# Kernel tuning notes

Measured on AMD Instinct MI355X. Metric: run time of the kernel, lower is better.

## Reference

```python
import jax, jax.numpy as jnp
import numpy as np
from jax import lax


def _dtw_normalized(x, y):
    """DTW with symmetric2 step pattern and cityblock (L1) local cost on scalars.

    D[0,0] = d[0,0]; D[i,0] = D[i-1,0] + d[i,0]; D[0,j] = D[0,j-1] + d[0,j]
    D[i,j] = min(D[i-1,j-1] + 2*d, D[i-1,j] + d, D[i,j-1] + d)
    normalizedDistance = D[n-1,m-1] / (n + m)
    """
    n = x.shape[0]

    def row_update(d_prev, xi):
        d = jnp.abs(xi - y)              # local cost row, [m]
        first = d_prev[0] + d[0]         # D[i,0]

        def step(left, inp):
            dj, up, diag = inp
            val = jnp.minimum(jnp.minimum(diag + 2.0 * dj, up + dj), left + dj)
            return val, val

        _, rest = lax.scan(step, first, (d[1:], d_prev[1:], d_prev[:-1]))
        new_row = jnp.concatenate([first[None], rest])
        return new_row, None

    d0 = jnp.cumsum(jnp.abs(x[0] - y))   # D[0, :]
    d_last, _ = lax.scan(row_update, d0, x[1:])
    return d_last[-1] / (2.0 * n)        # n + m with n == m


def setup_inputs() -> dict:
    key = jax.random.key(0)
    k1, k2 = jax.random.split(key)
    x = jax.random.normal(k1, (64, 1024), dtype=jnp.float32)
    x_target = jax.random.normal(k2, (64, 1024), dtype=jnp.float32)
    return {"x": x, "x_target": x_target}


def reference(x, x_target):
    dists = jax.vmap(_dtw_normalized)(x, x_target)  # [bs]
    return jnp.mean(dists)
```

## Files before the change

kernel.cpp:

```cpp
#include <hip/hip_runtime.h>

#define SEQ_N 1024
#define BATCH 64
#define NW    4
#define RPL   4
#define KSL   16
#define DELTA (64 + KSL)
#define RINGN 80
#define PAD_F 304
#define PAD_B 352

__device__ __forceinline__ float wave_shr1(float v, float fill) {
    return __int_as_float(__builtin_amdgcn_update_dpp(
        __float_as_int(fill), __float_as_int(v), 0x138, 0xF, 0xF, false));
}

__global__ __launch_bounds__(256, 1) void dtw_kernel(const float* __restrict__ x,
                                                     const float* __restrict__ y,
                                                     float* __restrict__ dists) {
    __shared__ float sy_raw[PAD_F + SEQ_N + PAD_B];
    __shared__ float ring[NW - 1][RINGN];

    const int b   = blockIdx.x;
    const int tid = threadIdx.x;
    const int w   = tid >> 6;
    const int l   = tid & 63;
    const float INF = 3.0e37f;
    const int  off = w * DELTA + l;
    const bool is_ring_l0 = (l == 0) && (w > 0);
    const bool is_tid0 = (tid == 0);

    for (int i = tid; i < PAD_F; i += 256) sy_raw[i] = 0.0f;
    for (int i = tid; i < PAD_B; i += 256) sy_raw[PAD_F + SEQ_N + i] = 0.0f;
    ((float4*)(sy_raw + PAD_F))[tid] = ((const float4*)(y + b * SEQ_N))[tid];
    const float4 xv = *((const float4*)(x + b * SEQ_N + w * 256 + l * RPL));
    const float xr0 = xv.x, xr1 = xv.y, xr2 = xv.z, xr3 = xv.w;
    __syncthreads();

    const float* const yp = sy_raw + PAD_F - off;

    float c0 = INF, c1 = INF, c2 = INF, c3 = INF;
    float diag_top = INF, bottom = INF;
    float yA[KSL], yB[KSL], rb[KSL], bt[KSL];

    #pragma unroll
    for (int k = 0; k < KSL; ++k) yA[k] = yp[k];

#define EPOCH(MASKED, FIRST, S0, YU, YF)                                     \
  {                                                                          \
    __syncthreads();                                                         \
    if (w > 0) {                                                             \
      int rbase = ((S0) & 63) + 47; if (rbase >= 64) rbase -= 64;            \
      const float* rp = ring[w - 1] + rbase;                                 \
      _Pragma("unroll")                                                      \
      for (int k2 = 0; k2 < KSL; ++k2) rb[k2] = rp[k2];                      \
    } else {                                                                 \
      _Pragma("unroll")                                                      \
      for (int k2 = 0; k2 < KSL; ++k2) rb[k2] = INF;                         \
    }                                                                        \
    _Pragma("unroll")                                                        \
    for (int k2 = 0; k2 < KSL; ++k2) YF[k2] = yp[(S0) + KSL + k2];           \
    _Pragma("unroll")                                                        \
    for (int k2 = 0; k2 < KSL; ++k2) {                                       \
      const float up_dpp = wave_shr1(bottom, INF);                           \
      float upv = is_ring_l0 ? rb[k2] : up_dpp;                              \
      if ((FIRST) && k2 == 0 && is_tid0) upv = 0.0f;      \
      const float yj = YU[k2];                                               \
      bool act = true;                                                       \
      if (MASKED) act = ((unsigned)((S0) + k2 - off) < (unsigned)SEQ_N);     \
      if (act) {                                                             \
        const float d0 = xr0 - yj, d1 = xr1 - yj,                            \
                    d2 = xr2 - yj, d3 = xr3 - yj;                            \
        const float t0 = diag_top + fabsf(d0);                               \
        const float t1 = c0 + fabsf(d1);                                     \
        const float t2 = c1 + fabsf(d2);                                     \
        const float t3 = c2 + fabsf(d3);                                     \
        float v = upv;                                                       \
        v = fminf(fminf(t0, c0), v) + fabsf(d0); c0 = v;                     \
        v = fminf(fminf(t1, c1), v) + fabsf(d1); c1 = v;                     \
        v = fminf(fminf(t2, c2), v) + fabsf(d2); c2 = v;                     \
        v = fminf(fminf(t3, c3), v) + fabsf(d3); c3 = v;                     \
        diag_top = upv; bottom = v;                                          \
      }                                                                      \
      if ((FIRST) && k2 == 0 && is_tid0) diag_top = INF; \
      bt[k2] = bottom;                                                       \
    }                                                                        \
    if (w < NW - 1 && l == 63) {                                             \
      const int mm = (S0) & 63;                                              \
      float* wp = ring[w] + mm;                                              \
      _Pragma("unroll")                                                      \
      for (int k2 = 0; k2 < KSL; ++k2) wp[k2] = bt[k2];                      \
      if (mm == 0) {                                                         \
        _Pragma("unroll")                                                    \
        for (int k2 = 0; k2 < KSL; ++k2) ring[w][64 + k2] = bt[k2];          \
      }                                                                      \
    }                                                                        \
  }

    EPOCH(true, true, 0, yA, yB);
    EPOCH(true, false, 16, yB, yA);
    int s0 = 32;
    for (int it = 1; it < 10; ++it) {
        EPOCH(true, false, s0, yA, yB);
        EPOCH(true, false, s0 + 16, yB, yA);
        s0 += 32;
    }
    for (int it = 0; it < 22; ++it) {
        EPOCH(false, false, s0, yA, yB);
        EPOCH(false, false, s0 + 16, yB, yA);
        s0 += 32;
    }
    for (int it = 0; it < 10; ++it) {
        EPOCH(true, false, s0, yA, yB);
        EPOCH(true, false, s0 + 16, yB, yA);
        s0 += 32;
    }
#undef EPOCH

    if (tid == 255) dists[b] = c3 * (1.0f / (2.0f * (float)SEQ_N));
}

__global__ void dtw_reduce_kernel(const float* __restrict__ dists,
                                  float* __restrict__ out) {
    float v = dists[threadIdx.x] * (1.0f / (float)BATCH);
    #pragma unroll
    for (int o = 32; o > 0; o >>= 1) v += __shfl_down(v, o);
    if (threadIdx.x == 0) out[0] = v;
}

extern "C" void kernel_launch(void* const* d_in, const int* in_sizes, int n_in,
                              void* d_out, int out_size, void* d_ws, size_t ws_size,
                              hipStream_t stream) {
    const float* x = (const float*)d_in[0];
    const float* y = (const float*)d_in[1];
    float* out = (float*)d_out;
    float* dists = (float*)d_ws;

    dtw_kernel<<<BATCH, 256, 0, stream>>>(x, y, dists);
    dtw_reduce_kernel<<<1, BATCH, 0, stream>>>(dists, out);
}
```

Baseline: 88.70 us.

## Double epoch length and stream ring exchange per step instead of batched

Raises the per-epoch step count from 16 to 32, halving the number of block-wide barriers, and widens the wavefront lag between waves to match. The batched ring reads and writes and the register prefetch of y are replaced by per-step LDS reads and writes into a 128-entry ring, with lane 63 writing each bottom value immediately. This trims register pressure and barrier count, at the cost of extra LDS accesses inside the serial dependency chain and a longer pipeline fill/drain.

```diff
diff --git a/kernel.cpp b/kernel.cpp
--- a/kernel.cpp
+++ b/kernel.cpp
@@ -4,10 +4,11 @@
 #define BATCH 64
 #define NW    4
 #define RPL   4
-#define KSL   16
-#define DELTA (64 + KSL)
-#define RINGN 80
-#define PAD_F 304
+#define KSL   32
+#define DELTA 96
+#define LAG   33
+#define RINGM 128
+#define PAD_F 352
 #define PAD_B 352
 
 __device__ __forceinline__ float wave_shr1(float v, float fill) {
@@ -19,7 +20,7 @@
                                                      const float* __restrict__ y,
                                                      float* __restrict__ dists) {
     __shared__ float sy_raw[PAD_F + SEQ_N + PAD_B];
-    __shared__ float ring[NW - 1][RINGN];
+    __shared__ float ring[NW - 1][RINGM];
 
     const int b   = blockIdx.x;
     const int tid = threadIdx.x;
@@ -27,7 +28,6 @@
     const int l   = tid & 63;
     const float INF = 3.0e37f;
     const int  off = w * DELTA + l;
-    const bool is_ring_l0 = (l == 0) && (w > 0);
     const bool is_tid0 = (tid == 0);
 
     for (int i = tid; i < PAD_F; i += 256) sy_raw[i] = 0.0f;
@@ -41,31 +41,22 @@
 
     float c0 = INF, c1 = INF, c2 = INF, c3 = INF;
     float diag_top = INF, bottom = INF;
-    float yA[KSL], yB[KSL], rb[KSL], bt[KSL];
 
-    #pragma unroll
-    for (int k = 0; k < KSL; ++k) yA[k] = yp[k];
-
-#define EPOCH(MASKED, FIRST, S0, YU, YF)                                     \
+#define EPOCH(MASKED, FIRST, S0)                                             \
   {                                                                          \
     __syncthreads();                                                         \
-    if (w > 0) {                                                             \
-      int rbase = ((S0) & 63) + 47; if (rbase >= 64) rbase -= 64;            \
-      const float* rp = ring[w - 1] + rbase;                                 \
-      _Pragma("unroll")                                                      \
-      for (int k2 = 0; k2 < KSL; ++k2) rb[k2] = rp[k2];                      \
-    } else {                                                                 \
-      _Pragma("unroll")                                                      \
-      for (int k2 = 0; k2 < KSL; ++k2) rb[k2] = INF;                         \
-    }                                                                        \
-    _Pragma("unroll")                                                        \
-    for (int k2 = 0; k2 < KSL; ++k2) YF[k2] = yp[(S0) + KSL + k2];           \
     _Pragma("unroll")                                                        \
     for (int k2 = 0; k2 < KSL; ++k2) {                                       \
       const float up_dpp = wave_shr1(bottom, INF);                           \
-      float upv = is_ring_l0 ? rb[k2] : up_dpp;                              \
+      float upv;                                                             \
+      if (w > 0) {                                                           \
+        const float rv = ring[w - 1][((S0) + k2 - LAG) & (RINGM - 1)];       \
+        upv = (l == 0) ? rv : up_dpp;                                        \
+      } else {                                                               \
+        upv = up_dpp;                                                        \
+      }                                                                      \
       if ((FIRST) && k2 == 0 && is_tid0) upv = 0.0f;      \
-      const float yj = YU[k2];                                               \
+      const float yj = yp[(S0) + k2];                                        \
       bool act = true;                                                       \
       if (MASKED) act = ((unsigned)((S0) + k2 - off) < (unsigned)SEQ_N);     \
       if (act) {                                                             \
@@ -83,38 +74,16 @@
         diag_top = upv; bottom = v;                                          \
       }                                                                      \
       if ((FIRST) && k2 == 0 && is_tid0) diag_top = INF; \
-      bt[k2] = bottom;                                                       \
-    }                                                                        \
-    if (w < NW - 1 && l == 63) {                                             \
-      const int mm = (S0) & 63;                                              \
-      float* wp = ring[w] + mm;                                              \
-      _Pragma("unroll")                                                      \
-      for (int k2 = 0; k2 < KSL; ++k2) wp[k2] = bt[k2];                      \
-      if (mm == 0) {                                                         \
-        _Pragma("unroll")                                                    \
-        for (int k2 = 0; k2 < KSL; ++k2) ring[w][64 + k2] = bt[k2];          \
-      }                                                                      \
+      if (w < NW - 1 && l == 63)                                             \
+        ring[w][((S0) + k2) & (RINGM - 1)] = bottom;                         \
     }                                                                        \
   }
 
-    EPOCH(true, true, 0, yA, yB);
-    EPOCH(true, false, 16, yB, yA);
-    int s0 = 32;
-    for (int it = 1; it < 10; ++it) {
-        EPOCH(true, false, s0, yA, yB);
-        EPOCH(true, false, s0 + 16, yB, yA);
-        s0 += 32;
-    }
-    for (int it = 0; it < 22; ++it) {
-        EPOCH(false, false, s0, yA, yB);
-        EPOCH(false, false, s0 + 16, yB, yA);
-        s0 += 32;
-    }
-    for (int it = 0; it < 10; ++it) {
-        EPOCH(true, false, s0, yA, yB);
-        EPOCH(true, false, s0 + 16, yB, yA);
-        s0 += 32;
-    }
+    int s0 = 0;
+    EPOCH(true, true, 0); s0 = 32;
+    for (int e = 1; e <= 10; ++e) { EPOCH(true, false, s0); s0 += 32; }
+    for (int e = 11; e <= 31; ++e) { EPOCH(false, false, s0); s0 += 32; }
+    for (int e = 32; e <= 42; ++e) { EPOCH(true, false, s0); s0 += 32; }
 #undef EPOCH
 
     if (tid == 255) dists[b] = c3 * (1.0f / (2.0f * (float)SEQ_N));
```

After: 195.7 us. +120.6%, slower.

## Process two DP columns per wavefront step to halve the anti-diagonal steps

Applied to the files above, without the earlier changes.

Each lane now computes two adjacent y-columns (a float2 pair) per step instead of one, so the wavefront sweeps 512 column pairs rather than 1024 columns. Shared y storage and the inter-wave ring buffer become float2, the epoch count drops by about half, and the masking uses the pair index. This cuts the number of DPP shifts, barriers and serial steps. The cost is a longer dependency chain inside each step (eight chained min-adds instead of four) and more registers.

```diff
diff --git a/kernel.cpp b/kernel.cpp
--- a/kernel.cpp
+++ b/kernel.cpp
@@ -3,12 +3,12 @@
 #define SEQ_N 1024
 #define BATCH 64
 #define NW    4
-#define RPL   4
 #define KSL   16
-#define DELTA (64 + KSL)
+#define DELTA 80
 #define RINGN 80
-#define PAD_F 304
-#define PAD_B 352
+#define PAD_F2 304
+#define PAD_B2 320
+#define NPAIR 512
 
 __device__ __forceinline__ float wave_shr1(float v, float fill) {
     return __int_as_float(__builtin_amdgcn_update_dpp(
@@ -18,8 +18,8 @@
 __global__ __launch_bounds__(256, 1) void dtw_kernel(const float* __restrict__ x,
                                                      const float* __restrict__ y,
                                                      float* __restrict__ dists) {
-    __shared__ float sy_raw[PAD_F + SEQ_N + PAD_B];
-    __shared__ float ring[NW - 1][RINGN];
+    __shared__ float2 sy2[PAD_F2 + NPAIR + PAD_B2];
+    __shared__ float2 ring[NW - 1][RINGN];
 
     const int b   = blockIdx.x;
     const int tid = threadIdx.x;
@@ -28,66 +28,77 @@
     const float INF = 3.0e37f;
     const int  off = w * DELTA + l;
     const bool is_ring_l0 = (l == 0) && (w > 0);
-    const bool is_tid0 = (tid == 0);
+    const bool is_seed = (tid == 0);
 
-    for (int i = tid; i < PAD_F; i += 256) sy_raw[i] = 0.0f;
-    for (int i = tid; i < PAD_B; i += 256) sy_raw[PAD_F + SEQ_N + i] = 0.0f;
-    ((float4*)(sy_raw + PAD_F))[tid] = ((const float4*)(y + b * SEQ_N))[tid];
-    const float4 xv = *((const float4*)(x + b * SEQ_N + w * 256 + l * RPL));
+    for (int i = tid; i < PAD_F2; i += 256) sy2[i] = make_float2(0.f, 0.f);
+    for (int i = tid; i < PAD_B2; i += 256) sy2[PAD_F2 + NPAIR + i] = make_float2(0.f, 0.f);
+    ((float4*)(sy2 + PAD_F2))[tid] = ((const float4*)(y + b * SEQ_N))[tid];
+    const float4 xv = *((const float4*)(x + b * SEQ_N + w * 256 + l * 4));
     const float xr0 = xv.x, xr1 = xv.y, xr2 = xv.z, xr3 = xv.w;
     __syncthreads();
 
-    const float* const yp = sy_raw + PAD_F - off;
+    const float2* const yp2 = sy2 + PAD_F2 - off;
 
     float c0 = INF, c1 = INF, c2 = INF, c3 = INF;
-    float diag_top = INF, bottom = INF;
-    float yA[KSL], yB[KSL], rb[KSL], bt[KSL];
+    float diag_top = INF;
+    float botA = INF, botB = INF;
+    float2 yA[KSL], yB[KSL], rb[KSL], bt[KSL];
 
     #pragma unroll
-    for (int k = 0; k < KSL; ++k) yA[k] = yp[k];
+    for (int k = 0; k < KSL; ++k) yA[k] = yp2[k];
+    #pragma unroll
+    for (int k = 0; k < KSL; ++k) rb[k] = make_float2(INF, INF);
 
 #define EPOCH(MASKED, FIRST, S0, YU, YF)                                     \
   {                                                                          \
     __syncthreads();                                                         \
     if (w > 0) {                                                             \
       int rbase = ((S0) & 63) + 47; if (rbase >= 64) rbase -= 64;            \
-      const float* rp = ring[w - 1] + rbase;                                 \
+      const float2* rp = ring[w - 1] + rbase;                                \
       _Pragma("unroll")                                                      \
       for (int k2 = 0; k2 < KSL; ++k2) rb[k2] = rp[k2];                      \
-    } else {                                                                 \
-      _Pragma("unroll")                                                      \
-      for (int k2 = 0; k2 < KSL; ++k2) rb[k2] = INF;                         \
     }                                                                        \
     _Pragma("unroll")                                                        \
-    for (int k2 = 0; k2 < KSL; ++k2) YF[k2] = yp[(S0) + KSL + k2];           \
+    for (int k2 = 0; k2 < KSL; ++k2) YF[k2] = yp2[(S0) + KSL + k2];          \
     _Pragma("unroll")                                                        \
     for (int k2 = 0; k2 < KSL; ++k2) {                                       \
-      const float up_dpp = wave_shr1(bottom, INF);                           \
-      float upv = is_ring_l0 ? rb[k2] : up_dpp;                              \
-      if ((FIRST) && k2 == 0 && is_tid0) upv = 0.0f;      \
-      const float yj = YU[k2];                                               \
+      float upA = wave_shr1(botA, INF);                                      \
+      float upB = wave_shr1(botB, INF);                                      \
+      if (is_ring_l0) { upA = rb[k2].x; upB = rb[k2].y; }                    \
+      const float dgB0 = upA;             \
+      if ((FIRST) && k2 == 0 && is_seed) upA = 0.0f;         \
+      const float2 yv = YU[k2];                                              \
       bool act = true;                                                       \
-      if (MASKED) act = ((unsigned)((S0) + k2 - off) < (unsigned)SEQ_N);     \
+      if (MASKED) act = ((unsigned)((S0) + k2 - off) < (unsigned)NPAIR);     \
       if (act) {                                                             \
-        const float d0 = xr0 - yj, d1 = xr1 - yj,                            \
-                    d2 = xr2 - yj, d3 = xr3 - yj;                            \
-        const float t0 = diag_top + fabsf(d0);                               \
-        const float t1 = c0 + fabsf(d1);                                     \
-        const float t2 = c1 + fabsf(d2);                                     \
-        const float t3 = c2 + fabsf(d3);                                     \
-        float v = upv;                                                       \
-        v = fminf(fminf(t0, c0), v) + fabsf(d0); c0 = v;                     \
-        v = fminf(fminf(t1, c1), v) + fabsf(d1); c1 = v;                     \
-        v = fminf(fminf(t2, c2), v) + fabsf(d2); c2 = v;                     \
-        v = fminf(fminf(t3, c3), v) + fabsf(d3); c3 = v;                     \
-        diag_top = upv; bottom = v;                                          \
+        const float dA0 = xr0 - yv.x, dA1 = xr1 - yv.x,                      \
+                    dA2 = xr2 - yv.x, dA3 = xr3 - yv.x;                      \
+        const float dB0 = xr0 - yv.y, dB1 = xr1 - yv.y,                      \
+                    dB2 = xr2 - yv.y, dB3 = xr3 - yv.y;                      \
+        const float tA0 = diag_top + fabsf(dA0);                             \
+        const float tA1 = c0 + fabsf(dA1);                                   \
+        const float tA2 = c1 + fabsf(dA2);                                   \
+        const float tA3 = c2 + fabsf(dA3);                                   \
+        const float a0 = fminf(fminf(tA0, c0), upA) + fabsf(dA0);            \
+        const float a1 = fminf(fminf(tA1, c1), a0) + fabsf(dA1);             \
+        const float a2 = fminf(fminf(tA2, c2), a1) + fabsf(dA2);             \
+        const float a3 = fminf(fminf(tA3, c3), a2) + fabsf(dA3);             \
+        const float tB0 = dgB0 + fabsf(dB0);                                 \
+        const float tB1 = a0 + fabsf(dB1);                                   \
+        const float tB2 = a1 + fabsf(dB2);                                   \
+        const float tB3 = a2 + fabsf(dB3);                                   \
+        const float b0 = fminf(fminf(tB0, a0), upB) + fabsf(dB0);            \
+        const float b1 = fminf(fminf(tB1, a1), b0) + fabsf(dB1);             \
+        const float b2 = fminf(fminf(tB2, a2), b1) + fabsf(dB2);             \
+        const float b3 = fminf(fminf(tB3, a3), b2) + fabsf(dB3);             \
+        c0 = b0; c1 = b1; c2 = b2; c3 = b3;                                  \
+        diag_top = upB; botA = a3; botB = b3;                                \
       }                                                                      \
-      if ((FIRST) && k2 == 0 && is_tid0) diag_top = INF; \
-      bt[k2] = bottom;                                                       \
+      bt[k2].x = botA; bt[k2].y = botB;                                      \
     }                                                                        \
     if (w < NW - 1 && l == 63) {                                             \
       const int mm = (S0) & 63;                                              \
-      float* wp = ring[w] + mm;                                              \
+      float2* wp = ring[w] + mm;                                             \
       _Pragma("unroll")                                                      \
       for (int k2 = 0; k2 < KSL; ++k2) wp[k2] = bt[k2];                      \
       if (mm == 0) {                                                         \
@@ -98,23 +109,24 @@
   }
 
     EPOCH(true, true, 0, yA, yB);
-    EPOCH(true, false, 16, yB, yA);
-    int s0 = 32;
-    for (int it = 1; it < 10; ++it) {
+    int s0 = 16;
+    for (int it = 0; it < 9; ++it) {
+        EPOCH(true, false, s0, yB, yA);
+        EPOCH(true, false, s0 + 16, yA, yB);
+        s0 += 32;
+    }
+    for (int it = 0; it < 6; ++it) {
+        EPOCH(false, false, s0, yB, yA);
+        EPOCH(false, false, s0 + 16, yA, yB);
+        s0 += 32;
+    }
+    EPOCH(false, false, s0, yB, yA); s0 += 16;
+    for (int it = 0; it < 9; ++it) {
         EPOCH(true, false, s0, yA, yB);
         EPOCH(true, false, s0 + 16, yB, yA);
         s0 += 32;
     }
-    for (int it = 0; it < 22; ++it) {
-        EPOCH(false, false, s0, yA, yB);
-        EPOCH(false, false, s0 + 16, yB, yA);
-        s0 += 32;
-    }
-    for (int it = 0; it < 10; ++it) {
-        EPOCH(true, false, s0, yA, yB);
-        EPOCH(true, false, s0 + 16, yB, yA);
-        s0 += 32;
-    }
+    EPOCH(true, false, s0, yA, yB);
 #undef EPOCH
 
     if (tid == 255) dists[b] = c3 * (1.0f / (2.0f * (float)SEQ_N));
```

Measured after the change: 93.58 us. +5.5%, slower.

## Split DTW into forward and backward half-sweeps meeting at middle column

Applied to the files above, without the earlier changes.

Each block now runs two DTW recurrences at once. One is a forward sweep over the first 512 columns, the other a backward sweep over the reversed sequences for the remaining columns. A new stitch kernel then combines the two boundary columns with a min over rows to recover the full-path cost. This halves the length of the serial anti-diagonal wavefront, which is the critical-path latency, but doubles the ALU work per epoch and adds an extra kernel launch plus workspace traffic. The backward recurrence carries extra local-cost state through the ring buffers, which adds register and LDS pressure.

```diff
diff --git a/kernel.cpp b/kernel.cpp
--- a/kernel.cpp
+++ b/kernel.cpp
@@ -3,23 +3,27 @@
 #define SEQ_N 1024
 #define BATCH 64
 #define NW    4
-#define RPL   4
 #define KSL   16
-#define DELTA (64 + KSL)
+#define DELTA 80
 #define RINGN 80
 #define PAD_F 304
-#define PAD_B 352
+#define PAD_B 320
+#define NPAIR 512
+#define SYN   (PAD_F + NPAIR + PAD_B)
 
 __device__ __forceinline__ float wave_shr1(float v, float fill) {
     return __int_as_float(__builtin_amdgcn_update_dpp(
         __float_as_int(fill), __float_as_int(v), 0x138, 0xF, 0xF, false));
 }
 
-__global__ __launch_bounds__(256, 1) void dtw_kernel(const float* __restrict__ x,
-                                                     const float* __restrict__ y,
-                                                     float* __restrict__ dists) {
-    __shared__ float sy_raw[PAD_F + SEQ_N + PAD_B];
-    __shared__ float ring[NW - 1][RINGN];
+__global__ __launch_bounds__(256, 1) void dtw_fused_kernel(const float* __restrict__ x,
+                                                           const float* __restrict__ y,
+                                                           float* __restrict__ wsF,
+                                                           float* __restrict__ wsP) {
+    __shared__ float  syF[SYN];
+    __shared__ float  syB[SYN];
+    __shared__ float  ringF[NW - 1][RINGN];
+    __shared__ float2 ringB[NW - 1][RINGN];
 
     const int b   = blockIdx.x;
     const int tid = threadIdx.x;
@@ -28,96 +32,174 @@
     const float INF = 3.0e37f;
     const int  off = w * DELTA + l;
     const bool is_ring_l0 = (l == 0) && (w > 0);
-    const bool is_tid0 = (tid == 0);
-
-    for (int i = tid; i < PAD_F; i += 256) sy_raw[i] = 0.0f;
-    for (int i = tid; i < PAD_B; i += 256) sy_raw[PAD_F + SEQ_N + i] = 0.0f;
-    ((float4*)(sy_raw + PAD_F))[tid] = ((const float4*)(y + b * SEQ_N))[tid];
-    const float4 xv = *((const float4*)(x + b * SEQ_N + w * 256 + l * RPL));
-    const float xr0 = xv.x, xr1 = xv.y, xr2 = xv.z, xr3 = xv.w;
+    const bool is_seed = (tid == 0);
+    const int  r0 = w * 256 + l * 4;
+
+    for (int i = tid; i < PAD_F; i += 256) { syF[i] = 0.0f; syB[i] = 0.0f; }
+    for (int i = tid; i < PAD_B; i += 256) {
+        syF[PAD_F + NPAIR + i] = 0.0f; syB[PAD_F + NPAIR + i] = 0.0f;
+    }
+    if (tid < NPAIR / 4) {
+        ((float4*)(syF + PAD_F))[tid] = ((const float4*)(y + b * SEQ_N))[tid];
+        const float4 v = *((const float4*)(y + b * SEQ_N + 1020 - 4 * tid));
+        ((float4*)(syB + PAD_F))[tid] = make_float4(v.w, v.z, v.y, v.x);
+    }
+    const float4 xf = *((const float4*)(x + b * SEQ_N + r0));
+    const float xF0 = xf.x, xF1 = xf.y, xF2 = xf.z, xF3 = xf.w;
+    const float4 xb = *((const float4*)(x + b * SEQ_N + 1020 - r0));
+    const float xB0 = xb.w, xB1 = xb.z, xB2 = xb.y, xB3 = xb.x;
     __syncthreads();
 
-    const float* const yp = sy_raw + PAD_F - off;
+    const float* const ypF = syF + PAD_F - off;
+    const float* const ypB = syB + PAD_F - off;
 
     float c0 = INF, c1 = INF, c2 = INF, c3 = INF;
-    float diag_top = INF, bottom = INF;
-    float yA[KSL], yB[KSL], rb[KSL], bt[KSL];
-
-    #pragma unroll
-    for (int k = 0; k < KSL; ++k) yA[k] = yp[k];
-
-#define EPOCH(MASKED, FIRST, S0, YU, YF)                                     \
+    float diag_top = INF, botF = INF;
+    float cP0 = INF, cP1 = INF, cP2 = INF, cP3 = INF;
+    float cD0 = 0.f, cD1 = 0.f, cD2 = 0.f, cD3 = 0.f;
+    float diag_P = INF, diag_D = 0.f, botP = INF, botD = 0.f;
+
+    float yFA[KSL], yFB[KSL], rbF[KSL], btF[KSL];
+    float yBA[KSL], yBB[KSL];
+    float2 rb2[KSL], bt2[KSL];
+
+    #pragma unroll
+    for (int k = 0; k < KSL; ++k) { yFA[k] = ypF[k]; yBA[k] = ypB[k]; }
+
+#define EPOCH(MASKED, FIRST, S0, YFU, YFF, YBU, YBF)                         \
   {                                                                          \
     __syncthreads();                                                         \
     if (w > 0) {                                                             \
       int rbase = ((S0) & 63) + 47; if (rbase >= 64) rbase -= 64;            \
-      const float* rp = ring[w - 1] + rbase;                                 \
+      const float*  rpF = ringF[w - 1] + rbase;                              \
+      const float2* rpB = ringB[w - 1] + rbase;                              \
       _Pragma("unroll")                                                      \
-      for (int k2 = 0; k2 < KSL; ++k2) rb[k2] = rp[k2];                      \
+      for (int k2 = 0; k2 < KSL; ++k2) { rbF[k2] = rpF[k2]; rb2[k2] = rpB[k2]; } \
     } else {                                                                 \
       _Pragma("unroll")                                                      \
-      for (int k2 = 0; k2 < KSL; ++k2) rb[k2] = INF;                         \
-    }                                                                        \
-    _Pragma("unroll")                                                        \
-    for (int k2 = 0; k2 < KSL; ++k2) YF[k2] = yp[(S0) + KSL + k2];           \
+      for (int k2 = 0; k2 < KSL; ++k2) {                                     \
+        rbF[k2] = INF; rb2[k2] = make_float2(INF, 0.f);                      \
+      }                                                                      \
+    }                                                                        \
     _Pragma("unroll")                                                        \
     for (int k2 = 0; k2 < KSL; ++k2) {                                       \
-      const float up_dpp = wave_shr1(bottom, INF);                           \
-      float upv = is_ring_l0 ? rb[k2] : up_dpp;                              \
-      if ((FIRST) && k2 == 0 && is_tid0) upv = 0.0f;      \
-      const float yj = YU[k2];                                               \
+      YFF[k2] = ypF[(S0) + KSL + k2]; YBF[k2] = ypB[(S0) + KSL + k2];        \
+    }                                                                        \
+    _Pragma("unroll")                                                        \
+    for (int k2 = 0; k2 < KSL; ++k2) {                                       \
+      float upF = wave_shr1(botF, INF);                                      \
+      float upP = wave_shr1(botP, INF);                                      \
+      float upD = wave_shr1(botD, 0.0f);                                     \
+      if (is_ring_l0) { upF = rbF[k2]; upP = rb2[k2].x; upD = rb2[k2].y; }   \
+      if ((FIRST) && k2 == 0 && is_seed) { upF = 0.0f; upP = 0.0f; }         \
+      const float yjF = YFU[k2];                                             \
+      const float yjB = YBU[k2];                                             \
       bool act = true;                                                       \
-      if (MASKED) act = ((unsigned)((S0) + k2 - off) < (unsigned)SEQ_N);     \
+      if (MASKED) act = ((unsigned)((S0) + k2 - off) < (unsigned)NPAIR);     \
       if (act) {                                                             \
-        const float d0 = xr0 - yj, d1 = xr1 - yj,                            \
-                    d2 = xr2 - yj, d3 = xr3 - yj;                            \
+                                                \
+        const float d0 = xF0 - yjF, d1 = xF1 - yjF,                          \
+                    d2 = xF2 - yjF, d3 = xF3 - yjF;                          \
         const float t0 = diag_top + fabsf(d0);                               \
         const float t1 = c0 + fabsf(d1);                                     \
         const float t2 = c1 + fabsf(d2);                                     \
         const float t3 = c2 + fabsf(d3);                                     \
-        float v = upv;                                                       \
+        float v = upF;                                                       \
         v = fminf(fminf(t0, c0), v) + fabsf(d0); c0 = v;                     \
         v = fminf(fminf(t1, c1), v) + fabsf(d1); c1 = v;                     \
         v = fminf(fminf(t2, c2), v) + fabsf(d2); c2 = v;                     \
         v = fminf(fminf(t3, c3), v) + fabsf(d3); c3 = v;                     \
-        diag_top = upv; bottom = v;                                          \
+        diag_top = upF; botF = v;                                            \
+                             \
+        const float f0 = xB0 - yjB, f1 = xB1 - yjB,                          \
+                    f2 = xB2 - yjB, f3 = xB3 - yjB;                          \
+        const float u0 = diag_P + fabsf(diag_D);                             \
+        const float u1 = cP0 + fabsf(cD0);                                   \
+        const float u2 = cP1 + fabsf(cD1);                                   \
+        const float u3 = cP2 + fabsf(cD2);                                   \
+        float Bv = fminf(fminf(u0, upP), cP0);                               \
+        const float P0 = Bv + fabsf(f0);                                     \
+        Bv = fminf(fminf(u1, P0), cP1); const float P1 = Bv + fabsf(f1);     \
+        Bv = fminf(fminf(u2, P1), cP2); const float P2 = Bv + fabsf(f2);     \
+        Bv = fminf(fminf(u3, P2), cP3); const float P3 = Bv + fabsf(f3);     \
+        cP0 = P0; cP1 = P1; cP2 = P2; cP3 = P3;                              \
+        cD0 = f0; cD1 = f1; cD2 = f2; cD3 = f3;                              \
+        diag_P = upP; diag_D = upD;                                          \
+        botP = P3; botD = f3;                                                \
       }                                                                      \
-      if ((FIRST) && k2 == 0 && is_tid0) diag_top = INF; \
-      bt[k2] = bottom;                                                       \
+      if ((FIRST) && k2 == 0 && is_seed) { diag_top = INF; diag_P = INF; }   \
+      btF[k2] = botF; bt2[k2] = make_float2(botP, botD);                     \
     }                                                                        \
     if (w < NW - 1 && l == 63) {                                             \
       const int mm = (S0) & 63;                                              \
-      float* wp = ring[w] + mm;                                              \
+      float*  wpF = ringF[w] + mm;                                           \
+      float2* wpB = ringB[w] + mm;                                           \
       _Pragma("unroll")                                                      \
-      for (int k2 = 0; k2 < KSL; ++k2) wp[k2] = bt[k2];                      \
+      for (int k2 = 0; k2 < KSL; ++k2) { wpF[k2] = btF[k2]; wpB[k2] = bt2[k2]; } \
       if (mm == 0) {                                                         \
         _Pragma("unroll")                                                    \
-        for (int k2 = 0; k2 < KSL; ++k2) ring[w][64 + k2] = bt[k2];          \
+        for (int k2 = 0; k2 < KSL; ++k2) {                                   \
+          ringF[w][64 + k2] = btF[k2]; ringB[w][64 + k2] = bt2[k2];          \
+        }                                                                    \
       }                                                                      \
     }                                                                        \
   }
 
-    EPOCH(true, true, 0, yA, yB);
-    EPOCH(true, false, 16, yB, yA);
-    int s0 = 32;
-    for (int it = 1; it < 10; ++it) {
-        EPOCH(true, false, s0, yA, yB);
-        EPOCH(true, false, s0 + 16, yB, yA);
+    EPOCH(true, true, 0, yFA, yFB, yBA, yBB);
+    int s0 = 16;
+    for (int it = 0; it < 9; ++it) {
+        EPOCH(true, false, s0, yFB, yFA, yBB, yBA);
+        EPOCH(true, false, s0 + 16, yFA, yFB, yBA, yBB);
         s0 += 32;
     }
-    for (int it = 0; it < 22; ++it) {
-        EPOCH(false, false, s0, yA, yB);
-        EPOCH(false, false, s0 + 16, yB, yA);
+    for (int it = 0; it < 6; ++it) {
+        EPOCH(false, false, s0, yFB, yFA, yBB, yBA);
+        EPOCH(false, false, s0 + 16, yFA, yFB, yBA, yBB);
         s0 += 32;
     }
-    for (int it = 0; it < 10; ++it) {
-        EPOCH(true, false, s0, yA, yB);
-        EPOCH(true, false, s0 + 16, yB, yA);
+    EPOCH(false, false, s0, yFB, yFA, yBB, yBA); s0 += 16;
+    for (int it = 0; it < 9; ++it) {
+        EPOCH(true, false, s0, yFA, yFB, yBA, yBB);
+        EPOCH(true, false, s0 + 16, yFB, yFA, yBB, yBA);
         s0 += 32;
     }
+    EPOCH(true, false, s0, yFA, yFB, yBA, yBB);
 #undef EPOCH
 
-    if (tid == 255) dists[b] = c3 * (1.0f / (2.0f * (float)SEQ_N));
+    *((float4*)(wsF + b * SEQ_N + r0)) = make_float4(c0, c1, c2, c3);
+    *((float4*)(wsP + b * SEQ_N + 1020 - r0)) = make_float4(cP3, cP2, cP1, cP0);
+}
+
+__global__ void dtw_stitch_kernel(const float* __restrict__ x,
+                                  const float* __restrict__ y,
+                                  const float* __restrict__ wsF,
+                                  const float* __restrict__ wsP,
+                                  float* __restrict__ dists) {
+    __shared__ float red[4];
+    const int b = blockIdx.x, t = threadIdx.x;
+    const float INF = 3.0e37f;
+    const float y512 = y[b * SEQ_N + 512];
+    const float4 Fv = ((const float4*)(wsF + b * SEQ_N))[t];
+    const float4 Pv = ((const float4*)(wsP + b * SEQ_N))[t];
+    const float Pn4 = (t < 255) ? wsP[b * SEQ_N + 4 * t + 4] : INF;
+    const float F[4]  = {Fv.x, Fv.y, Fv.z, Fv.w};
+    const float P[4]  = {Pv.x, Pv.y, Pv.z, Pv.w};
+    const float Pn[4] = {Pv.y, Pv.z, Pv.w, Pn4};
+    float m = INF;
+    #pragma unroll
+    for (int k = 0; k < 4; ++k) {
+        const int i = 4 * t + k;
+        const float xn = (i < 1023) ? x[b * SEQ_N + i + 1] : 0.f;
+        const float alt = (i < 1023) ? Pn[k] + fabsf(xn - y512) : INF;
+        m = fminf(m, F[k] + fminf(P[k], alt));
+    }
+    #pragma unroll
+    for (int o = 32; o > 0; o >>= 1) m = fminf(m, __shfl_down(m, o));
+    if ((t & 63) == 0) red[t >> 6] = m;
+    __syncthreads();
+    if (t == 0)
+        dists[b] = fminf(fminf(red[0], red[1]), fminf(red[2], red[3]))
+                   * (1.0f / (2.0f * (float)SEQ_N));
 }
 
 __global__ void dtw_reduce_kernel(const float* __restrict__ dists,
@@ -134,8 +216,11 @@
     const float* x = (const float*)d_in[0];
     const float* y = (const float*)d_in[1];
     float* out = (float*)d_out;
-    float* dists = (float*)d_ws;
-
-    dtw_kernel<<<BATCH, 256, 0, stream>>>(x, y, dists);
+    float* wsF   = (float*)d_ws;
+    float* wsP   = wsF + BATCH * SEQ_N;
+    float* dists = wsP + BATCH * SEQ_N;
+
+    dtw_fused_kernel<<<BATCH, 256, 0, stream>>>(x, y, wsF, wsP);
+    dtw_stitch_kernel<<<BATCH, 256, 0, stream>>>(x, y, wsF, wsP, dists);
     dtw_reduce_kernel<<<1, BATCH, 0, stream>>>(dists, out);
 }
```

Result: slower. 124.0 us (+39.8%).
